# Kernel tuning notes

Measured on AMD Instinct MI355X. Metric: run time of the kernel, lower is better.

## Reference

```python
import jax, jax.numpy as jnp
import numpy as np

N = 6144
IN_DIM = 512
CHANNELS = 4
C_DIM = 64
ITERATIONS = 3
BETA = 1.0
EDGE_P = 0.005  # ~30 avg degree


def _l2norm(x):
    # F.normalize(dim=-1): x / max(||x||_2, eps)
    return x / jnp.maximum(jnp.linalg.norm(x, axis=-1, keepdims=True), 1e-12)


def setup_inputs() -> dict:
    key = jax.random.key(0)
    kf, ka, kw, kb = jax.random.split(key, 4)
    features = jax.random.normal(kf, (N, IN_DIM), dtype=jnp.float32)
    # sparse 0/1 adjacency, densified (module calls adj.to_dense())
    adj = (jax.random.uniform(ka, (N, N)) < EDGE_P).astype(jnp.int32)
    # per-channel weights/biases, init ~ N(0, 1) as in init_parameters
    W = jax.random.normal(kw, (CHANNELS, IN_DIM, C_DIM), dtype=jnp.float32)
    b = jax.random.normal(kb, (CHANNELS, 1, C_DIM), dtype=jnp.float32)
    return {"features": features, "adj": adj, "W": W, "b": b}


def reference(features, adj, W, b):
    mask = adj > 0  # [N, N]
    # per-channel projection + row L2-normalize -> [C, N, K]
    feats = _l2norm(jnp.einsum('nd,cdk->cnk', features, W) + b)
    for _ in range(ITERATIONS):
        # per-channel dense self-attention scores, masked by adjacency
        att = jnp.einsum('cnk,cmk->cnm', feats, feats) / BETA  # [C, N, N]
        att = jnp.where(mask[None, :, :], att, 0.0)
        # softmax across channels (torch dim=2 after cat == channel axis)
        att = jax.nn.softmax(att, axis=0)
        att = jnp.where(mask[None, :, :], att, 0.0)
        # aggregate and renormalize
        feats = _l2norm(feats + jnp.einsum('cnm,cmk->cnk', att, feats))
    # concat channels along feature dim -> [N, C*K]
    return jnp.transpose(feats, (1, 0, 2)).reshape(N, CHANNELS * C_DIM)
```

## Files before the change

### kernel.cpp

```cpp
#include <hip/hip_runtime.h>
#include <hip/hip_bf16.h>
#include <math.h>

#define NN      6144
#define IN_DIM  512
#define CH      4
#define CDIM    64
#define NODE    256
#define PR      8
#define PBLK    (NN / PR)
#define MAXD    96

typedef int v4i __attribute__((ext_vector_type(4)));

__device__ __forceinline__ unsigned short f2bf(float x) {
    union { float f; unsigned int u; } v; v.f = x;
    const unsigned int r = v.u + 0x7FFFu + ((v.u >> 16) & 1u);
    return (unsigned short)(r >> 16);
}
__device__ __forceinline__ float bflo(unsigned int u) {
    union { unsigned int u; float f; } v; v.u = u << 16; return v.f;
}
__device__ __forceinline__ float bfhi(unsigned int u) {
    union { unsigned int u; float f; } v; v.u = u & 0xFFFF0000u; return v.f;
}
__device__ __forceinline__ void unpack8(uint4 u, float* o) {
    o[0] = bflo(u.x); o[1] = bfhi(u.x);
    o[2] = bflo(u.y); o[3] = bfhi(u.y);
    o[4] = bflo(u.z); o[5] = bfhi(u.z);
    o[6] = bflo(u.w); o[7] = bfhi(u.w);
}

template <int CTRL>
__device__ __forceinline__ float dppadd(float v) {
    return v + __int_as_float(
        __builtin_amdgcn_update_dpp(0, __float_as_int(v), CTRL, 0xF, 0xF, true));
}

__global__ __launch_bounds__(256) void proj_ell_kernel(
    const float* __restrict__ feat,
    const float* __restrict__ W,
    const float* __restrict__ bias,
    const int*   __restrict__ adj,
    unsigned short* __restrict__ outbf,
    int*   __restrict__ deg,
    int*   __restrict__ cols)
{
    __shared__ float lds[PR * IN_DIM];
    const int t = threadIdx.x;

    if (blockIdx.x < PBLK) {
        const int row0 = blockIdx.x * PR;
        {
            const float4* src = (const float4*)(feat + (size_t)row0 * IN_DIM);
            float4* dst = (float4*)lds;
#pragma unroll
            for (int i = 0; i < (PR * IN_DIM / 4) / 256; ++i)
                dst[t + i * 256] = src[t + i * 256];
        }
        __syncthreads();

        const int g  = t >> 6;
        const int q  = t & 63;
        const int c  = q >> 4;
        const int k0 = (q & 15) * 4;

        float acc[2][4];
#pragma unroll
        for (int r = 0; r < 2; ++r)
#pragma unroll
            for (int j = 0; j < 4; ++j) acc[r][j] = 0.0f;

        const float* Wc   = W + (size_t)c * IN_DIM * CDIM + k0;
        const float* arow = lds + g * 2 * IN_DIM;

        for (int d = 0; d < IN_DIM; d += 4) {
            const float4 w0 = *(const float4*)(Wc + (size_t)(d + 0) * CDIM);
            const float4 w1 = *(const float4*)(Wc + (size_t)(d + 1) * CDIM);
            const float4 w2 = *(const float4*)(Wc + (size_t)(d + 2) * CDIM);
            const float4 w3 = *(const float4*)(Wc + (size_t)(d + 3) * CDIM);
#pragma unroll
            for (int r = 0; r < 2; ++r) {
                const float4 a = *(const float4*)(arow + r * IN_DIM + d);
                acc[r][0] = fmaf(a.x, w0.x, fmaf(a.y, w1.x, fmaf(a.z, w2.x, fmaf(a.w, w3.x, acc[r][0]))));
                acc[r][1] = fmaf(a.x, w0.y, fmaf(a.y, w1.y, fmaf(a.z, w2.y, fmaf(a.w, w3.y, acc[r][1]))));
                acc[r][2] = fmaf(a.x, w0.z, fmaf(a.y, w1.z, fmaf(a.z, w2.z, fmaf(a.w, w3.z, acc[r][2]))));
                acc[r][3] = fmaf(a.x, w0.w, fmaf(a.y, w1.w, fmaf(a.z, w2.w, fmaf(a.w, w3.w, acc[r][3]))));
            }
        }

        const float4 bv = *(const float4*)(bias + c * CDIM + k0);
#pragma unroll
        for (int r = 0; r < 2; ++r) {
            acc[r][0] += bv.x; acc[r][1] += bv.y; acc[r][2] += bv.z; acc[r][3] += bv.w;
            float ss = acc[r][0] * acc[r][0] + acc[r][1] * acc[r][1]
                     + acc[r][2] * acc[r][2] + acc[r][3] * acc[r][3];
            ss += __shfl_xor(ss, 1, 64);
            ss += __shfl_xor(ss, 2, 64);
            ss += __shfl_xor(ss, 4, 64);
            ss += __shfl_xor(ss, 8, 64);
            const float rn = __builtin_amdgcn_rsqf(fmaxf(ss, 1e-24f));
            ushort4 res;
            res.x = f2bf(acc[r][0] * rn); res.y = f2bf(acc[r][1] * rn);
            res.z = f2bf(acc[r][2] * rn); res.w = f2bf(acc[r][3] * rn);
            *(ushort4*)(outbf + (size_t)(row0 + g * 2 + r) * NODE + c * CDIM + k0) = res;
        }
    } else {
        int* cnt = (int*)lds;
        const int n = blockIdx.x - PBLK;
        if (t == 0) *cnt = 0;
        __syncthreads();

        const v4i* row = (const v4i*)(adj + (size_t)n * NN);
        int* rowcols = cols + (size_t)n * MAXD;
        for (int i = t; i < NN / 4; i += 256) {
            const v4i v = __builtin_nontemporal_load(&row[i]);
            if (v.x | v.y | v.z | v.w) {
                const int base = i * 4;
                if (v.x) { int p = atomicAdd(cnt, 1); if (p < MAXD) rowcols[p] = base + 0; }
                if (v.y) { int p = atomicAdd(cnt, 1); if (p < MAXD) rowcols[p] = base + 1; }
                if (v.z) { int p = atomicAdd(cnt, 1); if (p < MAXD) rowcols[p] = base + 2; }
                if (v.w) { int p = atomicAdd(cnt, 1); if (p < MAXD) rowcols[p] = base + 3; }
            }
        }
        __syncthreads();
        if (t == 0) deg[n] = min(*cnt, MAXD);
    }
}

template <bool LAST>
__global__ __launch_bounds__(256) void iter_kernel(
    const unsigned short* __restrict__ fin,
    unsigned short* __restrict__ fout,
    float* __restrict__ fout32,
    const int* __restrict__ deg,
    const int* __restrict__ cols)
{
    const int wv   = threadIdx.x >> 6;
    const int lane = threadIdx.x & 63;
    const int n    = blockIdx.x * 4 + wv;
    const int nb   = lane >> 4;
    const int cj   = lane & 15;

    float qv[16], av[16];
    {
        const uint4* qp = (const uint4*)(fin + (size_t)n * NODE + cj * 16);
        unpack8(qp[0], qv); unpack8(qp[1], qv + 8);
    }
#pragma unroll
    for (int i = 0; i < 16; ++i) av[i] = 0.0f;

    const int d = deg[n];
    const int* cl = cols + (size_t)n * MAXD;
    const int nch = (d + 3) >> 2;

    bool val = nb < d;
    uint4 fa, fb;
    {
        const int m = val ? cl[nb] : 0;
        const uint4* fp = (const uint4*)(fin + (size_t)m * NODE + cj * 16);
        fa = fp[0]; fb = fp[1];
    }

    for (int ch = 0; ch < nch; ++ch) {
        const bool more = (ch + 1 < nch);
        bool valn = false;
        uint4 ga, gb;
        if (more) {
            const int idx = (ch + 1) * 4 + nb;
            valn = idx < d;
            const int m2 = valn ? cl[idx] : 0;
            const uint4* gp = (const uint4*)(fin + (size_t)m2 * NODE + cj * 16);
            ga = gp[0]; gb = gp[1];
        }

        float fv[16];
        unpack8(fa, fv); unpack8(fb, fv + 8);

        float p = 0.0f;
#pragma unroll
        for (int i = 0; i < 16; ++i) p = fmaf(qv[i], fv[i], p);
        p = dppadd<0xB1>(p);
        p = dppadd<0x4E>(p);
        const float e = __expf(p);
        float s = dppadd<0x124>(e);
        s = dppadd<0x128>(s);
        const float w = val ? e * __builtin_amdgcn_rcpf(s) : 0.0f;

#pragma unroll
        for (int i = 0; i < 16; ++i) av[i] = fmaf(w, fv[i], av[i]);

        if (more) { fa = ga; fb = gb; val = valn; }
    }

#pragma unroll
    for (int i = 0; i < 16; ++i) {
        av[i] += __shfl_xor(av[i], 16, 64);
        av[i] += __shfl_xor(av[i], 32, 64);
    }
#pragma unroll
    for (int i = 0; i < 16; ++i) av[i] += qv[i];

    float ss = 0.0f;
#pragma unroll
    for (int i = 0; i < 16; ++i) ss = fmaf(av[i], av[i], ss);
    ss = dppadd<0xB1>(ss);
    ss = dppadd<0x4E>(ss);
    const float rn = __builtin_amdgcn_rsqf(fmaxf(ss, 1e-24f));

    const float4 s0 = make_float4(av[0]  * rn, av[1]  * rn, av[2]  * rn, av[3]  * rn);
    const float4 s1 = make_float4(av[4]  * rn, av[5]  * rn, av[6]  * rn, av[7]  * rn);
    const float4 s2 = make_float4(av[8]  * rn, av[9]  * rn, av[10] * rn, av[11] * rn);
    const float4 s3 = make_float4(av[12] * rn, av[13] * rn, av[14] * rn, av[15] * rn);
    const float4 o = (nb == 0) ? s0 : (nb == 1) ? s1 : (nb == 2) ? s2 : s3;

    if (LAST) {
        *(float4*)(fout32 + (size_t)n * NODE + cj * 16 + nb * 4) = o;
    } else {
        ushort4 ob;
        ob.x = f2bf(o.x); ob.y = f2bf(o.y); ob.z = f2bf(o.z); ob.w = f2bf(o.w);
        *(ushort4*)(fout + (size_t)n * NODE + cj * 16 + nb * 4) = ob;
    }
}

extern "C" void kernel_launch(void* const* d_in, const int* in_sizes, int n_in,
                              void* d_out, int out_size, void* d_ws, size_t ws_size,
                              hipStream_t stream) {
    const float* features = (const float*)d_in[0];
    const int*   adj      = (const int*)d_in[1];
    const float* W        = (const float*)d_in[2];
    const float* b        = (const float*)d_in[3];
    float* out = (float*)d_out;

    unsigned short* featsA = (unsigned short*)d_ws;
    unsigned short* featsB = featsA + (size_t)NN * NODE;
    int* deg  = (int*)(featsB + (size_t)NN * NODE);
    int* cols = deg + NN;

    proj_ell_kernel<<<PBLK + NN, 256, 0, stream>>>(features, W, b, adj,
                                                   featsA, deg, cols);
    iter_kernel<false><<<NN / 4, 256, 0, stream>>>(featsA, featsB, nullptr, deg, cols);
    iter_kernel<false><<<NN / 4, 256, 0, stream>>>(featsB, featsA, nullptr, deg, cols);
    iter_kernel<true ><<<NN / 4, 256, 0, stream>>>(featsA, nullptr, out, deg, cols);
}
```

Measured before the change: 294.0 us.

## Fuse three attention iterations into one cooperative kernel with grid syncs

Replaces the three separate iteration kernel launches with a single cooperative kernel of 1024 blocks. Each block processes six nodes per iteration, and grid-wide syncs separate the iterations. This is meant to remove launch gaps and per-kernel ramp-up and tail costs. In exchange it adds grid barrier overhead and lower parallelism per phase, and it keeps the multi-kernel path as a fallback if the cooperative launch fails.

Measured after the change: 742.1 us. 2.52x slower.

```diff
diff --git a/kernel.cpp b/kernel.cpp
--- a/kernel.cpp
+++ b/kernel.cpp
@@ -1,6 +1,9 @@
 #include <hip/hip_runtime.h>
 #include <hip/hip_bf16.h>
+#include <hip/hip_cooperative_groups.h>
 #include <math.h>
+
+namespace cg = cooperative_groups;
 
 #define NN      6144
 #define IN_DIM  512
@@ -10,6 +13,8 @@
 #define PR      8
 #define PBLK    (NN / PR)
 #define MAXD    96
+#define FBLK    1024
+#define NPB     (NN / FBLK)
 
 typedef int v4i __attribute__((ext_vector_type(4)));
 
@@ -129,19 +134,14 @@
 }
 
 template <bool LAST>
-__global__ __launch_bounds__(256) void iter_kernel(
+__device__ __forceinline__ void iter_node(
     const unsigned short* __restrict__ fin,
     unsigned short* __restrict__ fout,
     float* __restrict__ fout32,
     const int* __restrict__ deg,
-    const int* __restrict__ cols)
-{
-    const int wv   = threadIdx.x >> 6;
-    const int lane = threadIdx.x & 63;
-    const int n    = blockIdx.x * 4 + wv;
-    const int nb   = lane >> 4;
-    const int cj   = lane & 15;
-
+    const int* __restrict__ cols,
+    const int n, const int nb, const int cj)
+{
     float qv[16], av[16];
     {
         const uint4* qp = (const uint4*)(fin + (size_t)n * NODE + cj * 16);
@@ -214,13 +214,55 @@
     const float4 s3 = make_float4(av[12] * rn, av[13] * rn, av[14] * rn, av[15] * rn);
     const float4 o = (nb == 0) ? s0 : (nb == 1) ? s1 : (nb == 2) ? s2 : s3;
 
-    if (LAST) {
+    if constexpr (LAST) {
         *(float4*)(fout32 + (size_t)n * NODE + cj * 16 + nb * 4) = o;
     } else {
         ushort4 ob;
         ob.x = f2bf(o.x); ob.y = f2bf(o.y); ob.z = f2bf(o.z); ob.w = f2bf(o.w);
         *(ushort4*)(fout + (size_t)n * NODE + cj * 16 + nb * 4) = ob;
     }
+}
+
+template <bool LAST>
+__global__ __launch_bounds__(256) void iter_kernel(
+    const unsigned short* __restrict__ fin,
+    unsigned short* __restrict__ fout,
+    float* __restrict__ fout32,
+    const int* __restrict__ deg,
+    const int* __restrict__ cols)
+{
+    const int wv   = threadIdx.x >> 6;
+    const int lane = threadIdx.x & 63;
+    iter_node<LAST>(fin, fout, fout32, deg, cols,
+                    blockIdx.x * 4 + wv, lane >> 4, lane & 15);
+}
+
+__global__ __launch_bounds__(256, 4) void fused_iter_kernel(
+    unsigned short* __restrict__ fA,
+    unsigned short* __restrict__ fB,
+    float* __restrict__ out,
+    const int* __restrict__ deg,
+    const int* __restrict__ cols)
+{
+    cg::grid_group grid = cg::this_grid();
+    const int wv   = threadIdx.x >> 6;
+    const int lane = threadIdx.x & 63;
+    const int nb   = lane >> 4;
+    const int cj   = lane & 15;
+    const int base = blockIdx.x * NPB;
+
+    for (int s = wv; s < NPB; s += 4)
+        iter_node<false>(fA, fB, nullptr, deg, cols, base + s, nb, cj);
+    __threadfence();
+    grid.sync();
+
+    for (int s = wv; s < NPB; s += 4)
+        iter_node<false>(fB, fA, nullptr, deg, cols, base + s, nb, cj);
+    __threadfence();
+    grid.sync();
+
+    for (int s = wv; s < NPB; s += 4)
+        iter_node<true>(fA, nullptr, out, deg, cols, base + s, nb, cj);
 }
 
 extern "C" void kernel_launch(void* const* d_in, const int* in_sizes, int n_in,
@@ -239,7 +281,17 @@
 
     proj_ell_kernel<<<PBLK + NN, 256, 0, stream>>>(features, W, b, adj,
                                                    featsA, deg, cols);
-    iter_kernel<false><<<NN / 4, 256, 0, stream>>>(featsA, featsB, nullptr, deg, cols);
-    iter_kernel<false><<<NN / 4, 256, 0, stream>>>(featsB, featsA, nullptr, deg, cols);
-    iter_kernel<true ><<<NN / 4, 256, 0, stream>>>(featsA, nullptr, out, deg, cols);
-}
+
+    {
+        void* args[] = { (void*)&featsA, (void*)&featsB, (void*)&out,
+                         (void*)&deg, (void*)&cols };
+        hipError_t e = hipLaunchCooperativeKernel((const void*)fused_iter_kernel,
+                                                  dim3(FBLK), dim3(256),
+                                                  args, 0, stream);
+        if (e != hipSuccess) {
+            iter_kernel<false><<<NN / 4, 256, 0, stream>>>(featsA, featsB, nullptr, deg, cols);
+            iter_kernel<false><<<NN / 4, 256, 0, stream>>>(featsB, featsA, nullptr, deg, cols);
+            iter_kernel<true ><<<NN / 4, 256, 0, stream>>>(featsA, nullptr, out, deg, cols);
+        }
+    }
+}
```
